# Performance work log

Measured on AMD Instinct MI355X. Metric: run time of the kernel, lower is better.

## Reference

```python
import jax, jax.numpy as jnp
import numpy as np

NUM_EXPERTS = 2
TOP_K = 2


def setup_inputs() -> dict:
    key = jax.random.key(0)
    ks = jax.random.split(key, 5)
    B, T, M, H, E = 8, 512, 2048, 1024, NUM_EXPERTS
    x = jax.random.normal(ks[0], (B, T, M), dtype=jnp.float32)
    wg = jax.random.normal(ks[1], (M, E), dtype=jnp.float32) * 0.02
    w1 = jax.random.normal(ks[2], (E, M, H), dtype=jnp.float32) * 0.02
    b1 = jnp.zeros((E, H), dtype=jnp.float32)
    w2 = jax.random.normal(ks[3], (E, H, M), dtype=jnp.float32) * 0.02
    b2 = jnp.zeros((E, M), dtype=jnp.float32)
    return {"x": x, "wg": wg, "w1": w1, "b1": b1, "w2": w2, "b2": b2}


def _moe_forward(x, wg, w1, b1, w2, b2):
    B, T, M = x.shape
    E = wg.shape[1]
    S = B * T
    C = TOP_K * ((S + E - 1) // E)  # GShard top-2 capacity, factor 1.0
    xf = x.reshape(S, M)

    # --- fp32 gate (Top2Gate) ---
    logits = jnp.einsum('sm,me->se', xf.astype(jnp.float32), wg.astype(jnp.float32))
    gates = jax.nn.softmax(logits, axis=-1)  # [S,E]

    idx1 = jnp.argmax(gates, axis=-1)
    mask1 = jax.nn.one_hot(idx1, E, dtype=jnp.float32)
    gates_wo1 = jnp.where(mask1 > 0, -jnp.inf, logits)
    idx2 = jnp.argmax(gates_wo1, axis=-1)
    mask2 = jax.nn.one_hot(idx2, E, dtype=jnp.float32)

    # positions within each expert's buffer
    loc1 = jnp.cumsum(mask1, axis=0) - 1.0                      # [S,E]
    loc2 = jnp.cumsum(mask2, axis=0) - 1.0 + jnp.sum(mask1, axis=0, keepdims=True)
    mask1 = mask1 * (loc1 < C)
    mask2 = mask2 * (loc2 < C)

    g1 = jnp.sum(gates * mask1, axis=1)  # [S]
    g2 = jnp.sum(gates * mask2, axis=1)
    denom = jnp.maximum(g1 + g2, jnp.finfo(jnp.float32).eps)
    g1, g2 = g1 / denom, g2 / denom

    p1 = jnp.sum(loc1 * mask1, axis=1).astype(jnp.int32)  # capacity slot per token
    p2 = jnp.sum(loc2 * mask2, axis=1).astype(jnp.int32)
    oh1 = jax.nn.one_hot(p1, C, dtype=jnp.float32)  # [S,C]
    oh2 = jax.nn.one_hot(p2, C, dtype=jnp.float32)

    combine = (g1[:, None, None] * mask1[:, :, None] * oh1[:, None, :]
               + g2[:, None, None] * mask2[:, :, None] * oh2[:, None, :])  # [S,E,C]
    dispatch = (combine > 0).astype(xf.dtype)

    # --- dispatch, grouped expert FFN, combine ---
    disp = jnp.einsum('sec,sm->ecm', dispatch, xf)                 # [E,C,M]
    h = jax.nn.relu(jnp.einsum('ecm,emh->ech', disp, w1) + b1[:, None, :])
    y = jnp.einsum('ech,ehm->ecm', h, w2) + b2[:, None, :]         # [E,C,M]
    out = jnp.einsum('sec,ecm->sm', combine.astype(xf.dtype), y)   # [S,M]
    return out.reshape(B, T, M)


def reference(x, wg, w1, b1, w2, b2):
    moe_out = _moe_forward(x, wg, w1, b1, w2, b2)          # [B,T,M]
    summed = jnp.sum(moe_out, axis=2)                      # [B,T]
    return jax.nn.log_softmax(summed, axis=1)
```

## Files before the change

kernel.cpp:

```cpp
#include <hip/hip_runtime.h>

typedef unsigned short u16;
typedef unsigned int   u32;
typedef u16   u16x4 __attribute__((ext_vector_type(4)));
typedef u16   u16x8 __attribute__((ext_vector_type(8)));
typedef short s16x8 __attribute__((ext_vector_type(8)));
typedef float f32x4 __attribute__((ext_vector_type(4)));

#define S_TOK 4096
#define MDIM  2048
#define NDIM  2048
#define HDIM  1024
#define TDIM  512

__device__ __forceinline__ u16 f2bf(float f) {
  u32 u = __float_as_uint(f);
  u = u + 0x7fffu + ((u >> 16) & 1u);
  return (u16)(u >> 16);
}

__device__ __forceinline__ void gl2lds16(const void* g, void* l) {
  __builtin_amdgcn_global_load_lds(
      (const __attribute__((address_space(1))) void*)g,
      (__attribute__((address_space(3))) void*)l, 16, 0, 0);
}

__global__ __launch_bounds__(256) void prep_all(const float* __restrict__ w1,
                                                u16* __restrict__ w1t,
                                                const float* __restrict__ w2,
                                                const float* __restrict__ b2,
                                                float* __restrict__ w2sum,
                                                float* __restrict__ b2sum,
                                                const float* __restrict__ x,
                                                const float* __restrict__ wg,
                                                float* __restrict__ g,
                                                u16* __restrict__ xbf,
                                                float* __restrict__ ssum) {
  __shared__ float tile[32][33];
  int b = blockIdx.x;
  int t = threadIdx.x;
  if (b < 4096) {
    int e   = b >> 11;
    int idx = b & 2047;
    int m0  = (idx >> 5) << 5;
    int h0  = (idx & 31) << 5;
    int r = t >> 3, q = t & 7;
    const float* src = w1 + ((size_t)e * MDIM + (m0 + r)) * HDIM + h0 + q * 4;
    f32x4 v = *(const f32x4*)src;
    tile[r][q*4+0] = v[0]; tile[r][q*4+1] = v[1];
    tile[r][q*4+2] = v[2]; tile[r][q*4+3] = v[3];
    __syncthreads();
    u16x4 o;
    o[0] = f2bf(tile[q*4+0][r]);
    o[1] = f2bf(tile[q*4+1][r]);
    o[2] = f2bf(tile[q*4+2][r]);
    o[3] = f2bf(tile[q*4+3][r]);
    u16* dst = w1t + ((size_t)e * HDIM + (h0 + r)) * MDIM + m0 + q * 4;
    *(u16x4*)dst = o;
  } else if (b < 4609) {
    int bid  = b - 4096;
    int row  = bid * 4 + (t >> 6);
    int lane = t & 63;
    const float* src;
    if (row < NDIM)          src = w2 + (size_t)row * MDIM;
    else if (row < NDIM + 2) src = b2 + (size_t)(row - NDIM) * MDIM;
    else return;
    float acc = 0.f;
    for (int m = lane * 4; m < MDIM; m += 256) {
      f32x4 v = *(const f32x4*)(src + m);
      acc += v[0] + v[1] + v[2] + v[3];
    }
    #pragma unroll
    for (int off = 32; off; off >>= 1) acc += __shfl_xor(acc, off);
    if (lane == 0) {
      if (row < NDIM) w2sum[row] = acc;
      else            b2sum[row - NDIM] = acc;
    }
  } else if (b == 4609) {
    f32x4 z = {0.f, 0.f, 0.f, 0.f};
    #pragma unroll
    for (int i = 0; i < 8; ++i)
      *(f32x4*)(ssum + (t + i * 256) * 4) = z;
  } else {
    int bid  = b - 4610;
    int s    = bid * 4 + (t >> 6);
    int lane = t & 63;
    const float* xr = x + (size_t)s * MDIM;
    u16* xbr = xbf + (size_t)s * MDIM;
    float l0 = 0.f, l1 = 0.f;
    for (int m = lane * 4; m < MDIM; m += 256) {
      f32x4 xv = *(const f32x4*)(xr + m);
      f32x4 wa = *(const f32x4*)(wg + 2 * m);
      f32x4 wb = *(const f32x4*)(wg + 2 * m + 4);
      l0 += xv[0]*wa[0] + xv[1]*wa[2] + xv[2]*wb[0] + xv[3]*wb[2];
      l1 += xv[0]*wa[1] + xv[1]*wa[3] + xv[2]*wb[1] + xv[3]*wb[3];
      u16x4 o; o[0]=f2bf(xv[0]); o[1]=f2bf(xv[1]); o[2]=f2bf(xv[2]); o[3]=f2bf(xv[3]);
      *(u16x4*)(xbr + m) = o;
    }
    #pragma unroll
    for (int off = 32; off; off >>= 1) {
      l0 += __shfl_xor(l0, off);
      l1 += __shfl_xor(l1, off);
    }
    if (lane == 0) {
      float mx = fmaxf(l0, l1);
      float e0 = expf(l0 - mx), e1 = expf(l1 - mx);
      float inv = 1.f / (e0 + e1);
      g[2*s]   = e0 * inv;
      g[2*s+1] = e1 * inv;
    }
  }
}

#define BM 128
#define BN 128
#define BK 64
#define KT (MDIM / BK)

#define MFMA_BF16 __builtin_amdgcn_mfma_f32_16x16x32_bf16

__global__ __launch_bounds__(256, 2) void gemm_fused(const u16* __restrict__ xbf,
                                                     const u16* __restrict__ w1t,
                                                     const float* __restrict__ b1,
                                                     const float* __restrict__ w2sum,
                                                     float* __restrict__ ssum) {
  __shared__ u16 As[2][BM * BK];
  __shared__ u16 Bs[2][BN * BK];

  int bid  = blockIdx.x;
  int tile = (bid & 7) * 64 + (bid >> 3);
  int bn = tile & 15;
  int bm = tile >> 4;
  int gs0 = bm * BM;
  int gn0 = bn * BN;

  int tid  = threadIdx.x;
  int lane = tid & 63;
  int wid  = tid >> 6;
  int wr = wid >> 1, wc = wid & 1;
  int fr = lane & 15, fg = lane >> 4;

  int lr = lane >> 3;
  int lc = (lane & 7) ^ lr;
  int row0 = wid * 32;
  const u16* aS = xbf + (size_t)(gs0 + row0 + lr) * MDIM + lc * 8;
  const u16* bS = w1t + (size_t)(gn0 + row0 + lr) * MDIM + lc * 8;
  int sD = row0 * BK;

  int ch0 = (fg ^ (fr & 7)) * 8;
  int aOff[4], bOff[4];
  #pragma unroll
  for (int i = 0; i < 4; ++i) aOff[i] = (wr * 64 + i * 16 + fr) * BK + ch0;
  #pragma unroll
  for (int j = 0; j < 4; ++j) bOff[j] = (wc * 64 + j * 16 + fr) * BK + ch0;

  f32x4 acc[4][4] = {};

  #pragma unroll
  for (int q = 0; q < 4; ++q) {
    gl2lds16(aS + q * 8 * MDIM, &As[0][sD + q * 8 * BK]);
    gl2lds16(bS + q * 8 * MDIM, &Bs[0][sD + q * 8 * BK]);
  }

  for (int t = 0; t < KT; ++t) {
    const u16* Ac = &As[t & 1][0];
    const u16* Bc = &Bs[t & 1][0];
    u16* An = &As[(t & 1) ^ 1][0];
    u16* Bn = &Bs[(t & 1) ^ 1][0];
    bool notlast = (t + 1 < KT);

    if (notlast) {
      int nk = (t + 1) * BK;
      #pragma unroll
      for (int q = 0; q < 4; ++q) {
        gl2lds16(aS + nk + q * 8 * MDIM, An + sD + q * 8 * BK);
        gl2lds16(bS + nk + q * 8 * MDIM, Bn + sD + q * 8 * BK);
      }
      asm volatile("s_waitcnt vmcnt(8)" ::: "memory");
    } else {
      asm volatile("s_waitcnt vmcnt(0)" ::: "memory");
    }
    __builtin_amdgcn_s_barrier();

    #pragma unroll
    for (int kk = 0; kk < 2; ++kk) {
      int x32 = kk * 32;
      s16x8 af[4], bf[4];
      #pragma unroll
      for (int i = 0; i < 4; ++i) af[i] = *(const s16x8*)(Ac + (aOff[i] ^ x32));
      #pragma unroll
      for (int j = 0; j < 4; ++j) bf[j] = *(const s16x8*)(Bc + (bOff[j] ^ x32));
      __builtin_amdgcn_s_setprio(1);
      #pragma unroll
      for (int i = 0; i < 4; ++i)
        #pragma unroll
        for (int j = 0; j < 4; ++j)
          acc[i][j] = MFMA_BF16(af[i], bf[j], acc[i][j], 0, 0, 0);
      __builtin_amdgcn_s_setprio(0);
    }

    __builtin_amdgcn_s_barrier();
  }

  int e = gn0 >> 10;
  float b1v[4], w2v[4];
  #pragma unroll
  for (int j = 0; j < 4; ++j) {
    int n = gn0 + wc * 64 + j * 16 + fr;
    b1v[j] = b1[n];
    w2v[j] = w2sum[n];
  }
  #pragma unroll
  for (int i = 0; i < 4; ++i) {
    #pragma unroll
    for (int r = 0; r < 4; ++r) {
      float sv = 0.f;
      #pragma unroll
      for (int j = 0; j < 4; ++j)
        sv += fmaxf(acc[i][j][r] + b1v[j], 0.f) * w2v[j];
      sv += __shfl_xor(sv, 1);
      sv += __shfl_xor(sv, 2);
      sv += __shfl_xor(sv, 4);
      sv += __shfl_xor(sv, 8);
      if (fr == 0) {
        int s = gs0 + wr * 64 + i * 16 + fg * 4 + r;
        atomicAdd(&ssum[(size_t)e * S_TOK + s], sv);
      }
    }
  }
}

__global__ __launch_bounds__(512) void finalize(const float* __restrict__ g,
                                                const float* __restrict__ ssum,
                                                const float* __restrict__ b2sum,
                                                float* __restrict__ out) {
  __shared__ float sA[8];
  __shared__ float sB[2];
  int b = blockIdx.x;
  int t = threadIdx.x;
  int s = b * TDIM + t;
  int lane = t & 63, wid = t >> 6;
  float g0 = g[2*s], g1 = g[2*s+1];
  float v = g0 * (ssum[s] + b2sum[0]) + g1 * (ssum[S_TOK + s] + b2sum[1]);
  float m = v;
  #pragma unroll
  for (int off = 32; off; off >>= 1) m = fmaxf(m, __shfl_xor(m, off));
  if (lane == 0) sA[wid] = m;
  __syncthreads();
  if (t == 0) {
    float mm = sA[0];
    #pragma unroll
    for (int i = 1; i < 8; ++i) mm = fmaxf(mm, sA[i]);
    sB[0] = mm;
  }
  __syncthreads();
  float gm = sB[0];
  float ex = expf(v - gm);
  float sum = ex;
  #pragma unroll
  for (int off = 32; off; off >>= 1) sum += __shfl_xor(sum, off);
  if (lane == 0) sA[wid] = sum;
  __syncthreads();
  if (t == 0) {
    float ss = 0.f;
    #pragma unroll
    for (int i = 0; i < 8; ++i) ss += sA[i];
    sB[1] = logf(ss);
  }
  __syncthreads();
  out[s] = v - gm - sB[1];
}

extern "C" void kernel_launch(void* const* d_in, const int* in_sizes, int n_in,
                              void* d_out, int out_size, void* d_ws, size_t ws_size,
                              hipStream_t stream) {
  const float* x  = (const float*)d_in[0];
  const float* wg = (const float*)d_in[1];
  const float* w1 = (const float*)d_in[2];
  const float* b1 = (const float*)d_in[3];
  const float* w2 = (const float*)d_in[4];
  const float* b2 = (const float*)d_in[5];
  float* out = (float*)d_out;

  char* ws = (char*)d_ws;
  u16*   w1t   = (u16*)ws;
  u16*   xbf   = (u16*)(ws + 8388608);
  float* ssum  = (float*)(ws + 25165824);
  float* gbuf  = (float*)(ws + 25198592);
  float* w2sum = (float*)(ws + 25231360);
  float* b2sum = (float*)(ws + 25239552);

  hipLaunchKernelGGL(prep_all,   dim3(5634), dim3(256), 0, stream,
                     w1, w1t, w2, b2, w2sum, b2sum, x, wg, gbuf, xbf, ssum);
  hipLaunchKernelGGL(gemm_fused, dim3(512),  dim3(256), 0, stream, xbf, w1t, b1, w2sum, ssum);
  hipLaunchKernelGGL(finalize,   dim3(8),    dim3(512), 0, stream, gbuf, ssum, b2sum, out);
}
```

Measured before the change: 62.00 us.

## Enlarge GEMM tile to 256x128 with 8 waves and phased load/MFMA schedule

The fused GEMM now uses 256x128 tiles with 512-thread blocks, halving the grid to 256 blocks. The K loop is unrolled into four barrier-delimited phases per K-block. Each phase issues LDS fragment reads and part of the next tile's global-to-LDS copies ahead of eight MFMAs, so memory traffic interleaves with compute. This aims to raise data reuse per block and hide load latency, at the cost of more barriers per K step and one block per CU with larger LDS use.

```diff
diff --git a/kernel.cpp b/kernel.cpp
--- a/kernel.cpp
+++ b/kernel.cpp
@@ -112,14 +112,64 @@
   }
 }
 
-#define BM 128
+#define BM 256
 #define BN 128
 #define BK 64
 #define KT (MDIM / BK)
 
 #define MFMA_BF16 __builtin_amdgcn_mfma_f32_16x16x32_bf16
 
-__global__ __launch_bounds__(256, 2) void gemm_fused(const u16* __restrict__ xbf,
+#define PH_OPEN  __builtin_amdgcn_s_barrier(); \
+                 asm volatile("s_waitcnt lgkmcnt(0)" ::: "memory"); \
+                 __builtin_amdgcn_sched_barrier(0);
+#define PH_CLOSE __builtin_amdgcn_s_barrier();
+
+#define MFMA8(A0, A1, R0, R1, B0_, B1_, B2_, B3_) \
+  __builtin_amdgcn_s_setprio(1); \
+  acc[R0][0] = MFMA_BF16(A0, B0_, acc[R0][0], 0, 0, 0); \
+  acc[R0][1] = MFMA_BF16(A0, B1_, acc[R0][1], 0, 0, 0); \
+  acc[R0][2] = MFMA_BF16(A0, B2_, acc[R0][2], 0, 0, 0); \
+  acc[R0][3] = MFMA_BF16(A0, B3_, acc[R0][3], 0, 0, 0); \
+  acc[R1][0] = MFMA_BF16(A1, B0_, acc[R1][0], 0, 0, 0); \
+  acc[R1][1] = MFMA_BF16(A1, B1_, acc[R1][1], 0, 0, 0); \
+  acc[R1][2] = MFMA_BF16(A1, B2_, acc[R1][2], 0, 0, 0); \
+  acc[R1][3] = MFMA_BF16(A1, B3_, acc[R1][3], 0, 0, 0); \
+  __builtin_amdgcn_s_setprio(0);
+
+#define KBLOCK(CUR, NXT, SK, DS) { \
+  const u16* Ac = &As[CUR][0]; const u16* Bc = &Bs[CUR][0]; \
+  u16* Ad = &As[NXT][0];       u16* Bd = &Bs[NXT][0]; \
+  s16x8 a0, a1, b0, b1, b2, b3, c0, c1; \
+   \
+  a0 = *(const s16x8*)(Ac + aOff0); a1 = *(const s16x8*)(Ac + aOff1); \
+  b0 = *(const s16x8*)(Bc + bOff0); b1 = *(const s16x8*)(Bc + bOff1); \
+  b2 = *(const s16x8*)(Bc + bOff2); b3 = *(const s16x8*)(Bc + bOff3); \
+  if (DS) { \
+    gl2lds16(aS + (SK),            Ad + aD); \
+    gl2lds16(aS + (SK) + 8 * MDIM, Ad + aD + 8 * BK); \
+    gl2lds16(aS + (SK) + 16 * MDIM, Ad + aD + 16 * BK); \
+  } \
+  PH_OPEN  MFMA8(a0, a1, 0, 1, b0, b1, b2, b3)  PH_CLOSE \
+   \
+  a0 = *(const s16x8*)(Ac + aOff2); a1 = *(const s16x8*)(Ac + aOff3); \
+  c0 = *(const s16x8*)(Bc + (bOff0 ^ 32)); c1 = *(const s16x8*)(Bc + (bOff1 ^ 32)); \
+  if (DS) { \
+    gl2lds16(aS + (SK) + 24 * MDIM, Ad + aD + 24 * BK); \
+    gl2lds16(bS + (SK),            Bd + bD); \
+    gl2lds16(bS + (SK) + 8 * MDIM, Bd + bD + 8 * BK); \
+  } \
+  PH_OPEN  MFMA8(a0, a1, 2, 3, b0, b1, b2, b3)  PH_CLOSE \
+   \
+  a0 = *(const s16x8*)(Ac + (aOff0 ^ 32)); a1 = *(const s16x8*)(Ac + (aOff1 ^ 32)); \
+  b2 = *(const s16x8*)(Bc + (bOff2 ^ 32)); b3 = *(const s16x8*)(Bc + (bOff3 ^ 32)); \
+  PH_OPEN  MFMA8(a0, a1, 0, 1, c0, c1, b2, b3)  PH_CLOSE \
+   \
+  a0 = *(const s16x8*)(Ac + (aOff2 ^ 32)); a1 = *(const s16x8*)(Ac + (aOff3 ^ 32)); \
+  asm volatile("s_waitcnt vmcnt(0)" ::: "memory"); \
+  PH_OPEN  MFMA8(a0, a1, 2, 3, c0, c1, b2, b3)  PH_CLOSE \
+}
+
+__global__ __launch_bounds__(512, 2) void gemm_fused(const u16* __restrict__ xbf,
                                                      const u16* __restrict__ w1t,
                                                      const float* __restrict__ b1,
                                                      const float* __restrict__ w2sum,
@@ -128,9 +178,9 @@
   __shared__ u16 Bs[2][BN * BK];
 
   int bid  = blockIdx.x;
-  int tile = (bid & 7) * 64 + (bid >> 3);
+  int tile = (bid & 7) * 32 + (bid >> 3);
+  int bm = tile >> 4;
   int bn = tile & 15;
-  int bm = tile >> 4;
   int gs0 = bm * BM;
   int gn0 = bn * BN;
 
@@ -142,64 +192,36 @@
 
   int lr = lane >> 3;
   int lc = (lane & 7) ^ lr;
-  int row0 = wid * 32;
-  const u16* aS = xbf + (size_t)(gs0 + row0 + lr) * MDIM + lc * 8;
-  const u16* bS = w1t + (size_t)(gn0 + row0 + lr) * MDIM + lc * 8;
-  int sD = row0 * BK;
+  const u16* aS = xbf + (size_t)(gs0 + wid * 32 + lr) * MDIM + lc * 8;
+  const u16* bS = w1t + (size_t)(gn0 + wid * 16 + lr) * MDIM + lc * 8;
+  int aD = (wid * 32) * BK;
+  int bD = (wid * 16) * BK;
 
   int ch0 = (fg ^ (fr & 7)) * 8;
-  int aOff[4], bOff[4];
-  #pragma unroll
-  for (int i = 0; i < 4; ++i) aOff[i] = (wr * 64 + i * 16 + fr) * BK + ch0;
-  #pragma unroll
-  for (int j = 0; j < 4; ++j) bOff[j] = (wc * 64 + j * 16 + fr) * BK + ch0;
+  int aOff0 = (wr * 64 +  0 + fr) * BK + ch0;
+  int aOff1 = (wr * 64 + 16 + fr) * BK + ch0;
+  int aOff2 = (wr * 64 + 32 + fr) * BK + ch0;
+  int aOff3 = (wr * 64 + 48 + fr) * BK + ch0;
+  int bOff0 = (wc * 64 +  0 + fr) * BK + ch0;
+  int bOff1 = (wc * 64 + 16 + fr) * BK + ch0;
+  int bOff2 = (wc * 64 + 32 + fr) * BK + ch0;
+  int bOff3 = (wc * 64 + 48 + fr) * BK + ch0;
 
   f32x4 acc[4][4] = {};
 
   #pragma unroll
-  for (int q = 0; q < 4; ++q) {
-    gl2lds16(aS + q * 8 * MDIM, &As[0][sD + q * 8 * BK]);
-    gl2lds16(bS + q * 8 * MDIM, &Bs[0][sD + q * 8 * BK]);
-  }
-
-  for (int t = 0; t < KT; ++t) {
-    const u16* Ac = &As[t & 1][0];
-    const u16* Bc = &Bs[t & 1][0];
-    u16* An = &As[(t & 1) ^ 1][0];
-    u16* Bn = &Bs[(t & 1) ^ 1][0];
-    bool notlast = (t + 1 < KT);
-
-    if (notlast) {
-      int nk = (t + 1) * BK;
-      #pragma unroll
-      for (int q = 0; q < 4; ++q) {
-        gl2lds16(aS + nk + q * 8 * MDIM, An + sD + q * 8 * BK);
-        gl2lds16(bS + nk + q * 8 * MDIM, Bn + sD + q * 8 * BK);
-      }
-      asm volatile("s_waitcnt vmcnt(8)" ::: "memory");
-    } else {
-      asm volatile("s_waitcnt vmcnt(0)" ::: "memory");
-    }
-    __builtin_amdgcn_s_barrier();
-
-    #pragma unroll
-    for (int kk = 0; kk < 2; ++kk) {
-      int x32 = kk * 32;
-      s16x8 af[4], bf[4];
-      #pragma unroll
-      for (int i = 0; i < 4; ++i) af[i] = *(const s16x8*)(Ac + (aOff[i] ^ x32));
-      #pragma unroll
-      for (int j = 0; j < 4; ++j) bf[j] = *(const s16x8*)(Bc + (bOff[j] ^ x32));
-      __builtin_amdgcn_s_setprio(1);
-      #pragma unroll
-      for (int i = 0; i < 4; ++i)
-        #pragma unroll
-        for (int j = 0; j < 4; ++j)
-          acc[i][j] = MFMA_BF16(af[i], bf[j], acc[i][j], 0, 0, 0);
-      __builtin_amdgcn_s_setprio(0);
-    }
-
-    __builtin_amdgcn_s_barrier();
+  for (int q = 0; q < 4; ++q)
+    gl2lds16(aS + q * 8 * MDIM, &As[0][aD + q * 8 * BK]);
+  #pragma unroll
+  for (int q = 0; q < 2; ++q)
+    gl2lds16(bS + q * 8 * MDIM, &Bs[0][bD + q * 8 * BK]);
+  asm volatile("s_waitcnt vmcnt(0)" ::: "memory");
+  __builtin_amdgcn_s_barrier();
+
+  #pragma unroll 1
+  for (int I = 0; I < KT / 2; ++I) {
+    KBLOCK(0, 1, (2 * I + 1) * BK, true)
+    KBLOCK(1, 0, (2 * I + 2) * BK, I + 1 < KT / 2)
   }
 
   int e = gn0 >> 10;
@@ -292,6 +314,6 @@
 
   hipLaunchKernelGGL(prep_all,   dim3(5634), dim3(256), 0, stream,
                      w1, w1t, w2, b2, w2sum, b2sum, x, wg, gbuf, xbf, ssum);
-  hipLaunchKernelGGL(gemm_fused, dim3(512),  dim3(256), 0, stream, xbf, w1t, b1, w2sum, ssum);
+  hipLaunchKernelGGL(gemm_fused, dim3(256),  dim3(512), 0, stream, xbf, w1t, b1, w2sum, ssum);
   hipLaunchKernelGGL(finalize,   dim3(8),    dim3(512), 0, stream, gbuf, ssum, b2sum, out);
 }
```

Measured after the change: 72.74 us. 1.17x slower.

## Split GEMM K-slices across wave pairs with LDS reduction in 512-thread blocks

Applied to the files above, without the earlier changes.

Doubles the workgroup to 8 waves: each pair of waves covers the same 64x64 output sub-tile, with each wave handling one half of the BK=64 slice (intra-K split). The two partial accumulators are reduced through LDS before the fused bias/ReLU/w2-sum epilogue, which only the kw=0 waves run. The goal is more waves per CU to hide MFMA and load latency. In exchange each wave does half the MFMA work per barrier, and the change adds an LDS reduction round-trip plus idle waves during the epilogue.

```diff
diff --git a/kernel.cpp b/kernel.cpp
--- a/kernel.cpp
+++ b/kernel.cpp
@@ -119,13 +119,12 @@
 
 #define MFMA_BF16 __builtin_amdgcn_mfma_f32_16x16x32_bf16
 
-__global__ __launch_bounds__(256, 2) void gemm_fused(const u16* __restrict__ xbf,
+__global__ __launch_bounds__(512, 4) void gemm_fused(const u16* __restrict__ xbf,
                                                      const u16* __restrict__ w1t,
                                                      const float* __restrict__ b1,
                                                      const float* __restrict__ w2sum,
                                                      float* __restrict__ ssum) {
-  __shared__ u16 As[2][BM * BK];
-  __shared__ u16 Bs[2][BN * BK];
+  __shared__ u16 SH[32768];
 
   int bid  = blockIdx.x;
   int tile = (bid & 7) * 64 + (bid >> 3);
@@ -137,94 +136,113 @@
   int tid  = threadIdx.x;
   int lane = tid & 63;
   int wid  = tid >> 6;
-  int wr = wid >> 1, wc = wid & 1;
+  int pair = wid >> 1;
+  int kw   = wid & 1;
+  int pr = pair >> 1, pc = pair & 1;
   int fr = lane & 15, fg = lane >> 4;
 
   int lr = lane >> 3;
   int lc = (lane & 7) ^ lr;
-  int row0 = wid * 32;
+  int row0 = wid * 16;
   const u16* aS = xbf + (size_t)(gs0 + row0 + lr) * MDIM + lc * 8;
   const u16* bS = w1t + (size_t)(gn0 + row0 + lr) * MDIM + lc * 8;
   int sD = row0 * BK;
 
-  int ch0 = (fg ^ (fr & 7)) * 8;
+  u16* A0 = SH;
+  u16* B0 = SH + 16384;
+
+  int ch = ((fg ^ (fr & 7)) * 8) ^ (kw * 32);
   int aOff[4], bOff[4];
   #pragma unroll
-  for (int i = 0; i < 4; ++i) aOff[i] = (wr * 64 + i * 16 + fr) * BK + ch0;
+  for (int i = 0; i < 4; ++i) aOff[i] = (pr * 64 + i * 16 + fr) * BK + ch;
   #pragma unroll
-  for (int j = 0; j < 4; ++j) bOff[j] = (wc * 64 + j * 16 + fr) * BK + ch0;
+  for (int j = 0; j < 4; ++j) bOff[j] = (pc * 64 + j * 16 + fr) * BK + ch;
 
   f32x4 acc[4][4] = {};
 
-  #pragma unroll
-  for (int q = 0; q < 4; ++q) {
-    gl2lds16(aS + q * 8 * MDIM, &As[0][sD + q * 8 * BK]);
-    gl2lds16(bS + q * 8 * MDIM, &Bs[0][sD + q * 8 * BK]);
-  }
+  gl2lds16(aS,            A0 + sD);
+  gl2lds16(aS + 8 * MDIM, A0 + sD + 8 * BK);
+  gl2lds16(bS,            B0 + sD);
+  gl2lds16(bS + 8 * MDIM, B0 + sD + 8 * BK);
 
   for (int t = 0; t < KT; ++t) {
-    const u16* Ac = &As[t & 1][0];
-    const u16* Bc = &Bs[t & 1][0];
-    u16* An = &As[(t & 1) ^ 1][0];
-    u16* Bn = &Bs[(t & 1) ^ 1][0];
+    const u16* Ac = A0 + (t & 1) * 8192;
+    const u16* Bc = B0 + (t & 1) * 8192;
+    u16* An = A0 + ((t & 1) ^ 1) * 8192;
+    u16* Bn = B0 + ((t & 1) ^ 1) * 8192;
     bool notlast = (t + 1 < KT);
 
     if (notlast) {
       int nk = (t + 1) * BK;
-      #pragma unroll
-      for (int q = 0; q < 4; ++q) {
-        gl2lds16(aS + nk + q * 8 * MDIM, An + sD + q * 8 * BK);
-        gl2lds16(bS + nk + q * 8 * MDIM, Bn + sD + q * 8 * BK);
-      }
-      asm volatile("s_waitcnt vmcnt(8)" ::: "memory");
+      gl2lds16(aS + nk,            An + sD);
+      gl2lds16(aS + nk + 8 * MDIM, An + sD + 8 * BK);
+      gl2lds16(bS + nk,            Bn + sD);
+      gl2lds16(bS + nk + 8 * MDIM, Bn + sD + 8 * BK);
+      asm volatile("s_waitcnt vmcnt(4)" ::: "memory");
     } else {
       asm volatile("s_waitcnt vmcnt(0)" ::: "memory");
     }
     __builtin_amdgcn_s_barrier();
 
-    #pragma unroll
-    for (int kk = 0; kk < 2; ++kk) {
-      int x32 = kk * 32;
-      s16x8 af[4], bf[4];
+    s16x8 af[4], bf[4];
+    #pragma unroll
+    for (int i = 0; i < 4; ++i) af[i] = *(const s16x8*)(Ac + aOff[i]);
+    #pragma unroll
+    for (int j = 0; j < 4; ++j) bf[j] = *(const s16x8*)(Bc + bOff[j]);
+    __builtin_amdgcn_s_setprio(1);
+    #pragma unroll
+    for (int i = 0; i < 4; ++i)
       #pragma unroll
-      for (int i = 0; i < 4; ++i) af[i] = *(const s16x8*)(Ac + (aOff[i] ^ x32));
+      for (int j = 0; j < 4; ++j)
+        acc[i][j] = MFMA_BF16(af[i], bf[j], acc[i][j], 0, 0, 0);
+    __builtin_amdgcn_s_setprio(0);
+
+    __builtin_amdgcn_s_barrier();
+  }
+
+  f32x4* LDSf = (f32x4*)SH;
+  if (kw) {
+    #pragma unroll
+    for (int i = 0; i < 4; ++i)
       #pragma unroll
-      for (int j = 0; j < 4; ++j) bf[j] = *(const s16x8*)(Bc + (bOff[j] ^ x32));
-      __builtin_amdgcn_s_setprio(1);
+      for (int j = 0; j < 4; ++j)
+        LDSf[pair * 1024 + (i * 4 + j) * 64 + lane] = acc[i][j];
+  }
+  __syncthreads();
+  if (!kw) {
+    #pragma unroll
+    for (int i = 0; i < 4; ++i)
       #pragma unroll
-      for (int i = 0; i < 4; ++i)
+      for (int j = 0; j < 4; ++j) {
+        f32x4 v = LDSf[pair * 1024 + (i * 4 + j) * 64 + lane];
+        acc[i][j][0] += v[0]; acc[i][j][1] += v[1];
+        acc[i][j][2] += v[2]; acc[i][j][3] += v[3];
+      }
+
+    int e = gn0 >> 10;
+    float b1v[4], w2v[4];
+    #pragma unroll
+    for (int j = 0; j < 4; ++j) {
+      int n = gn0 + pc * 64 + j * 16 + fr;
+      b1v[j] = b1[n];
+      w2v[j] = w2sum[n];
+    }
+    #pragma unroll
+    for (int i = 0; i < 4; ++i) {
+      #pragma unroll
+      for (int r = 0; r < 4; ++r) {
+        float sv = 0.f;
         #pragma unroll
         for (int j = 0; j < 4; ++j)
-          acc[i][j] = MFMA_BF16(af[i], bf[j], acc[i][j], 0, 0, 0);
-      __builtin_amdgcn_s_setprio(0);
-    }
-
-    __builtin_amdgcn_s_barrier();
-  }
-
-  int e = gn0 >> 10;
-  float b1v[4], w2v[4];
-  #pragma unroll
-  for (int j = 0; j < 4; ++j) {
-    int n = gn0 + wc * 64 + j * 16 + fr;
-    b1v[j] = b1[n];
-    w2v[j] = w2sum[n];
-  }
-  #pragma unroll
-  for (int i = 0; i < 4; ++i) {
-    #pragma unroll
-    for (int r = 0; r < 4; ++r) {
-      float sv = 0.f;
-      #pragma unroll
-      for (int j = 0; j < 4; ++j)
-        sv += fmaxf(acc[i][j][r] + b1v[j], 0.f) * w2v[j];
-      sv += __shfl_xor(sv, 1);
-      sv += __shfl_xor(sv, 2);
-      sv += __shfl_xor(sv, 4);
-      sv += __shfl_xor(sv, 8);
-      if (fr == 0) {
-        int s = gs0 + wr * 64 + i * 16 + fg * 4 + r;
-        atomicAdd(&ssum[(size_t)e * S_TOK + s], sv);
+          sv += fmaxf(acc[i][j][r] + b1v[j], 0.f) * w2v[j];
+        sv += __shfl_xor(sv, 1);
+        sv += __shfl_xor(sv, 2);
+        sv += __shfl_xor(sv, 4);
+        sv += __shfl_xor(sv, 8);
+        if (fr == 0) {
+          int s = gs0 + pr * 64 + i * 16 + fg * 4 + r;
+          atomicAdd(&ssum[(size_t)e * S_TOK + s], sv);
+        }
       }
     }
   }
@@ -292,6 +310,6 @@
 
   hipLaunchKernelGGL(prep_all,   dim3(5634), dim3(256), 0, stream,
                      w1, w1t, w2, b2, w2sum, b2sum, x, wg, gbuf, xbf, ssum);
-  hipLaunchKernelGGL(gemm_fused, dim3(512),  dim3(256), 0, stream, xbf, w1t, b1, w2sum, ssum);
+  hipLaunchKernelGGL(gemm_fused, dim3(512),  dim3(512), 0, stream, xbf, w1t, b1, w2sum, ssum);
   hipLaunchKernelGGL(finalize,   dim3(8),    dim3(512), 0, stream, gbuf, ssum, b2sum, out);
 }
```

Result: slower. 65.60 us (+5.8%).

## Use 256-row tiles with 8 waves and triple-buffered LDS prefetch

Applied to the files above, without the earlier changes.

The fused GEMM now uses 256x128 output tiles computed by 512-thread blocks (8 waves), halving the grid to 256 blocks. B tiles of w1 are therefore fetched half as often per output element. The LDS pipeline moves from double to triple buffering with a prefetch distance of two stages. This removes the trailing barrier, so each k-iteration has a single barrier. The cost is much larger LDS use, about 147 KB per block, which limits each CU to one block. It also launches only one block per CU, with less freedom to hide tail latency.

```diff
diff --git a/kernel.cpp b/kernel.cpp
--- a/kernel.cpp
+++ b/kernel.cpp
@@ -112,25 +112,27 @@
   }
 }
 
-#define BM 128
+#define BM 256
 #define BN 128
 #define BK 64
 #define KT (MDIM / BK)
+#define ASZ (BM * BK)
+#define BSZ (BN * BK)
 
 #define MFMA_BF16 __builtin_amdgcn_mfma_f32_16x16x32_bf16
 
-__global__ __launch_bounds__(256, 2) void gemm_fused(const u16* __restrict__ xbf,
+__global__ __launch_bounds__(512, 2) void gemm_fused(const u16* __restrict__ xbf,
                                                      const u16* __restrict__ w1t,
                                                      const float* __restrict__ b1,
                                                      const float* __restrict__ w2sum,
                                                      float* __restrict__ ssum) {
-  __shared__ u16 As[2][BM * BK];
-  __shared__ u16 Bs[2][BN * BK];
+  __shared__ u16 As[3 * ASZ];
+  __shared__ u16 Bs[3 * BSZ];
 
   int bid  = blockIdx.x;
-  int tile = (bid & 7) * 64 + (bid >> 3);
+  int tile = (bid & 7) * 32 + (bid >> 3);
+  int bm = tile >> 4;
   int bn = tile & 15;
-  int bm = tile >> 4;
   int gs0 = bm * BM;
   int gn0 = bn * BN;
 
@@ -142,10 +144,10 @@
 
   int lr = lane >> 3;
   int lc = (lane & 7) ^ lr;
-  int row0 = wid * 32;
-  const u16* aS = xbf + (size_t)(gs0 + row0 + lr) * MDIM + lc * 8;
-  const u16* bS = w1t + (size_t)(gn0 + row0 + lr) * MDIM + lc * 8;
-  int sD = row0 * BK;
+  const u16* aS = xbf + (size_t)(gs0 + wid * 32 + lr) * MDIM + lc * 8;
+  const u16* bS = w1t + (size_t)(gn0 + wid * 16 + lr) * MDIM + lc * 8;
+  int aD = (wid * 32) * BK;
+  int bD = (wid * 16) * BK;
 
   int ch0 = (fg ^ (fr & 7)) * 8;
   int aOff[4], bOff[4];
@@ -157,31 +159,38 @@
   f32x4 acc[4][4] = {};
 
   #pragma unroll
-  for (int q = 0; q < 4; ++q) {
-    gl2lds16(aS + q * 8 * MDIM, &As[0][sD + q * 8 * BK]);
-    gl2lds16(bS + q * 8 * MDIM, &Bs[0][sD + q * 8 * BK]);
-  }
-
+  for (int tt = 0; tt < 2; ++tt) {
+    int k0 = tt * BK;
+    u16* Ad = &As[tt * ASZ];
+    u16* Bd = &Bs[tt * BSZ];
+    #pragma unroll
+    for (int q = 0; q < 4; ++q)
+      gl2lds16(aS + k0 + q * 8 * MDIM, Ad + aD + q * 8 * BK);
+    #pragma unroll
+    for (int q = 0; q < 2; ++q)
+      gl2lds16(bS + k0 + q * 8 * MDIM, Bd + bD + q * 8 * BK);
+  }
+
+  int cur = 0, wrt = 2;
   for (int t = 0; t < KT; ++t) {
-    const u16* Ac = &As[t & 1][0];
-    const u16* Bc = &Bs[t & 1][0];
-    u16* An = &As[(t & 1) ^ 1][0];
-    u16* Bn = &Bs[(t & 1) ^ 1][0];
-    bool notlast = (t + 1 < KT);
-
-    if (notlast) {
-      int nk = (t + 1) * BK;
-      #pragma unroll
-      for (int q = 0; q < 4; ++q) {
-        gl2lds16(aS + nk + q * 8 * MDIM, An + sD + q * 8 * BK);
-        gl2lds16(bS + nk + q * 8 * MDIM, Bn + sD + q * 8 * BK);
-      }
-      asm volatile("s_waitcnt vmcnt(8)" ::: "memory");
-    } else {
-      asm volatile("s_waitcnt vmcnt(0)" ::: "memory");
-    }
+    if (t + 1 < KT) asm volatile("s_waitcnt vmcnt(6)" ::: "memory");
+    else            asm volatile("s_waitcnt vmcnt(0)" ::: "memory");
     __builtin_amdgcn_s_barrier();
 
+    if (t + 2 < KT) {
+      int nk = (t + 2) * BK;
+      u16* Ad = &As[wrt * ASZ];
+      u16* Bd = &Bs[wrt * BSZ];
+      #pragma unroll
+      for (int q = 0; q < 4; ++q)
+        gl2lds16(aS + nk + q * 8 * MDIM, Ad + aD + q * 8 * BK);
+      #pragma unroll
+      for (int q = 0; q < 2; ++q)
+        gl2lds16(bS + nk + q * 8 * MDIM, Bd + bD + q * 8 * BK);
+    }
+
+    const u16* Ac = &As[cur * ASZ];
+    const u16* Bc = &Bs[cur * BSZ];
     #pragma unroll
     for (int kk = 0; kk < 2; ++kk) {
       int x32 = kk * 32;
@@ -199,7 +208,8 @@
       __builtin_amdgcn_s_setprio(0);
     }
 
-    __builtin_amdgcn_s_barrier();
+    cur = (cur == 2) ? 0 : cur + 1;
+    wrt = (wrt == 2) ? 0 : wrt + 1;
   }
 
   int e = gn0 >> 10;
@@ -292,6 +302,6 @@
 
   hipLaunchKernelGGL(prep_all,   dim3(5634), dim3(256), 0, stream,
                      w1, w1t, w2, b2, w2sum, b2sum, x, wg, gbuf, xbf, ssum);
-  hipLaunchKernelGGL(gemm_fused, dim3(512),  dim3(256), 0, stream, xbf, w1t, b1, w2sum, ssum);
+  hipLaunchKernelGGL(gemm_fused, dim3(256),  dim3(512), 0, stream, xbf, w1t, b1, w2sum, ssum);
   hipLaunchKernelGGL(finalize,   dim3(8),    dim3(512), 0, stream, gbuf, ssum, b2sum, out);
 }
```

New measurement: 68.90 us (median of 3 runs). 11.1% more time.
